# Optimization experiments

Hardware: AMD Instinct MI355X
Metric: run time of the kernel (lower is better)

The kernel has to match this reference:

```python
import jax, jax.numpy as jnp
import numpy as np

T, B, D_IN, D_H = 1024, 128, 256, 256


def setup_inputs() -> dict:
    key = jax.random.key(0)
    ks = jax.random.split(key, 9)
    s_in = 1.0 / np.sqrt(D_IN + D_H)  # torch nn.Linear init scale
    inputs = jax.random.normal(ks[0], (T, B, D_IN), dtype=jnp.float32)
    def lin(kw, kb):
        W = jax.random.uniform(kw, (D_IN + D_H, D_H), jnp.float32, -s_in, s_in)
        b = jax.random.uniform(kb, (D_H,), jnp.float32, -s_in, s_in)
        return W, b
    Wf, bf = lin(ks[1], ks[2])
    Wi, bi = lin(ks[3], ks[4])
    Wg, bg = lin(ks[5], ks[6])
    Wo, bo = lin(ks[7], ks[8])
    return {"inputs": inputs, "Wf": Wf, "bf": bf, "Wi": Wi, "bi": bi,
            "Wg": Wg, "bg": bg, "Wo": Wo, "bo": bo}


def reference(inputs, Wf, bf, Wi, bi, Wg, bg, Wo, bo):
    Bsz = inputs.shape[1]
    h0 = jnp.zeros((Bsz, D_H), inputs.dtype)
    c0 = jnp.zeros((Bsz, D_H), inputs.dtype)

    def step(carry, x):
        hx, cx = carry
        combined = jnp.concatenate([x, hx], axis=1)  # [B, D_IN+D_H]
        f = jax.nn.sigmoid(combined @ Wf + bf)
        i = jax.nn.sigmoid(combined @ Wi + bi)
        g = jnp.tanh(combined @ Wg + bg)
        o = jax.nn.sigmoid(combined @ Wo + bo)
        cx = f * cx + i * g
        hx = o * jnp.tanh(cx)
        return (hx, cx), hx

    (hx, cx), outputs = jax.lax.scan(step, (h0, c0), inputs)
    return outputs, (hx, cx)
```

## Files before the change

### kernel.cpp

```cpp
#include <hip/hip_runtime.h>
#include <hip/hip_bf16.h>

typedef short s16x8 __attribute__((ext_vector_type(8)));
typedef int   i32x4 __attribute__((ext_vector_type(4)));
typedef float f32x4 __attribute__((ext_vector_type(4)));
typedef float f32x2 __attribute__((ext_vector_type(2)));

#define T_STEPS 1024
#define BATCH   128
#define DIN     256
#define DH      256
#define NWG     64
#define NTHREADS 256

static __device__ __forceinline__ short f2bf(float f) {
  return __builtin_bit_cast(short, (__bf16)f);
}
static __device__ __forceinline__ float sigf(float x) {
  return 1.f / (1.f + __expf(-x));
}
static __device__ __forceinline__ float tanhfast(float x) {
  return 1.f - 2.f / (1.f + __expf(2.f * x));
}

static __device__ __forceinline__ i32x4 gload16_cc(const void* p) {
  i32x4 r;
  asm volatile("global_load_dwordx4 %0, %1, off sc0 sc1" : "=v"(r) : "v"(p));
  return r;
}
static __device__ __forceinline__ void gstore4_cc(void* p, unsigned v) {
  asm volatile("global_store_dword %0, %1, off sc0 sc1" :: "v"(p), "v"(v) : "memory");
}
static __device__ __forceinline__ void waitvm0_fence() {
  asm volatile("s_waitcnt vmcnt(0)" ::: "memory");
  __builtin_amdgcn_sched_barrier(0);
}

__global__ __launch_bounds__(NTHREADS, 1)
void lstm_rc(const float* __restrict__ X,
             const float* __restrict__ Wf, const float* __restrict__ bfv,
             const float* __restrict__ Wi, const float* __restrict__ biv,
             const float* __restrict__ Wg, const float* __restrict__ bgv,
             const float* __restrict__ Wo, const float* __restrict__ bov,
             float* __restrict__ out,
             unsigned short* __restrict__ hbuf,
             unsigned int* __restrict__ flags,
             int needEnd)
{
  const int bid = blockIdx.x;
  const int r   = bid & 7;
  const int csl = bid >> 3;
  const int tid = threadIdx.x;
  const int lane = tid & 63, wv = tid >> 6;
  const int grp = lane >> 4, l15 = lane & 15;
  const int r0 = r * 16;

  __shared__ short a_lds[2 * 32 * 16 * 8];
  __shared__ float elds[16 * 132];

  s16x8 bfr[2][16];
  {
    const float* Wm[4] = {Wf, Wi, Wg, Wo};
    const int gate = l15 >> 2, jj = l15 & 3;
    const float* Wsrc = Wm[gate];
#pragma unroll
    for (int n2 = 0; n2 < 2; ++n2) {
      const int ntg = wv * 2 + n2;
      const int hc  = csl * 32 + ntg * 4 + jj;
#pragma unroll
      for (int kk = 0; kk < 16; ++kk) {
        const float* p = Wsrc + (size_t)(kk * 32 + grp * 8) * DH + hc;
        s16x8 f;
#pragma unroll
        for (int s = 0; s < 8; ++s) f[s] = f2bf(p[(size_t)s * DH]);
        bfr[n2][kk] = f;
      }
    }
  }

  const int erow = tid >> 4;
  const int j2   = tid & 15;
  const int ntl  = j2 >> 1;
  const int jjl  = (j2 & 1) * 2;
  float bia[4][2];
  {
    const float* Bv[4] = {bfv, biv, bgv, bov};
#pragma unroll
    for (int g = 0; g < 4; ++g) {
      bia[g][0] = Bv[g][csl * 32 + 2 * j2];
      bia[g][1] = Bv[g][csl * 32 + 2 * j2 + 1];
    }
  }

  const int xrow = tid & 15, xseg = tid >> 4;

  f32x4 xp0, xp1, xp2, xp3;
  {
    const float* xs = X + ((size_t)0 * BATCH + r0 + xrow) * DIN + xseg * 16;
    f32x4 a = *(const f32x4*)xs, b = *(const f32x4*)(xs + 4);
    f32x4 cc = *(const f32x4*)(xs + 8), d = *(const f32x4*)(xs + 12);
    s16x8 lo, hi;
    lo[0]=f2bf(a[0]); lo[1]=f2bf(a[1]); lo[2]=f2bf(a[2]); lo[3]=f2bf(a[3]);
    lo[4]=f2bf(b[0]); lo[5]=f2bf(b[1]); lo[6]=f2bf(b[2]); lo[7]=f2bf(b[3]);
    hi[0]=f2bf(cc[0]);hi[1]=f2bf(cc[1]);hi[2]=f2bf(cc[2]);hi[3]=f2bf(cc[3]);
    hi[4]=f2bf(d[0]); hi[5]=f2bf(d[1]); hi[6]=f2bf(d[2]); hi[7]=f2bf(d[3]);
    *(s16x8*)&a_lds[((2 * xseg + 0) * 16 + xrow) * 8] = lo;
    *(s16x8*)&a_lds[((2 * xseg + 1) * 16 + xrow) * 8] = hi;
    const float* xn = X + ((size_t)1 * BATCH + r0 + xrow) * DIN + xseg * 16;
    xp0 = *(const f32x4*)xn;       xp1 = *(const f32x4*)(xn + 4);
    xp2 = *(const f32x4*)(xn + 8); xp3 = *(const f32x4*)(xn + 12);
  }
  __syncthreads();

  unsigned int* myflag = &flags[r * 32 + csl * 4 + wv];
  const unsigned int* pollp = &flags[r * 32 + (lane & 31)];
  float cs0 = 0.f, cs1 = 0.f, hO0 = 0.f, hO1 = 0.f;

  for (int t = 0; t < T_STEPS; ++t) {
    while (true) {
      unsigned fv = __hip_atomic_load(pollp, __ATOMIC_RELAXED,
                                      __HIP_MEMORY_SCOPE_AGENT);
      if (__all((int)(fv >= (unsigned)t))) break;
    }

    const unsigned short* hb = hbuf + (size_t)(t & 1) * (BATCH * DH);
    const unsigned short* hr = hb + (size_t)(r0 + l15) * DH + grp * 8;
    i32x4 hraw[8];
#pragma unroll
    for (int q = 0; q < 8; ++q) hraw[q] = gload16_cc(hr + q * 32);

    {
      short* ab = a_lds + ((t + 1) & 1) * (32 * 16 * 8);
      s16x8 lo, hi;
      lo[0]=f2bf(xp0[0]); lo[1]=f2bf(xp0[1]); lo[2]=f2bf(xp0[2]); lo[3]=f2bf(xp0[3]);
      lo[4]=f2bf(xp1[0]); lo[5]=f2bf(xp1[1]); lo[6]=f2bf(xp1[2]); lo[7]=f2bf(xp1[3]);
      hi[0]=f2bf(xp2[0]); hi[1]=f2bf(xp2[1]); hi[2]=f2bf(xp2[2]); hi[3]=f2bf(xp2[3]);
      hi[4]=f2bf(xp3[0]); hi[5]=f2bf(xp3[1]); hi[6]=f2bf(xp3[2]); hi[7]=f2bf(xp3[3]);
      *(s16x8*)&ab[((2 * xseg + 0) * 16 + xrow) * 8] = lo;
      *(s16x8*)&ab[((2 * xseg + 1) * 16 + xrow) * 8] = hi;
    }

    const short* ar = a_lds + (t & 1) * (32 * 16 * 8);
    f32x4 accx0 = {0.f,0.f,0.f,0.f}, accx1 = {0.f,0.f,0.f,0.f};
#pragma unroll
    for (int kk = 0; kk < 8; ++kk) {
      s16x8 a = *(const s16x8*)&ar[((kk * 4 + grp) * 16 + l15) * 8];
      accx0 = __builtin_amdgcn_mfma_f32_16x16x32_bf16(a, bfr[0][kk], accx0, 0, 0, 0);
      accx1 = __builtin_amdgcn_mfma_f32_16x16x32_bf16(a, bfr[1][kk], accx1, 0, 0, 0);
    }

    waitvm0_fence();
    f32x4 acch0 = {0.f,0.f,0.f,0.f}, acch1 = {0.f,0.f,0.f,0.f};
#pragma unroll
    for (int q = 0; q < 8; ++q) {
      s16x8 ah = __builtin_bit_cast(s16x8, hraw[q]);
      acch0 = __builtin_amdgcn_mfma_f32_16x16x32_bf16(ah, bfr[0][8 + q], acch0, 0, 0, 0);
      acch1 = __builtin_amdgcn_mfma_f32_16x16x32_bf16(ah, bfr[1][8 + q], acch1, 0, 0, 0);
    }
    f32x4 acc0 = accx0 + acch0, acc1 = accx1 + acch1;

    {
      const int tpre = (t + 2 < T_STEPS) ? t + 2 : T_STEPS - 1;
      const float* xs = X + ((size_t)tpre * BATCH + r0 + xrow) * DIN + xseg * 16;
      xp0 = *(const f32x4*)xs;       xp1 = *(const f32x4*)(xs + 4);
      xp2 = *(const f32x4*)(xs + 8); xp3 = *(const f32x4*)(xs + 12);
    }

#pragma unroll
    for (int rr = 0; rr < 4; ++rr) {
      elds[(grp * 4 + rr) * 132 + (wv * 2 + 0) * 16 + l15] = acc0[rr];
      elds[(grp * 4 + rr) * 132 + (wv * 2 + 1) * 16 + l15] = acc1[rr];
    }
    __syncthreads();

    const float* ez = &elds[erow * 132 + ntl * 16];
    float h0, h1;
    {
      float zf = ez[0 + jjl]  + bia[0][0];
      float zi = ez[4 + jjl]  + bia[1][0];
      float zg = ez[8 + jjl]  + bia[2][0];
      float zo = ez[12 + jjl] + bia[3][0];
      float cn = sigf(zf) * cs0 + sigf(zi) * tanhfast(zg);
      h0 = sigf(zo) * tanhfast(cn);
      cs0 = cn; hO0 = h0;
    }
    {
      float zf = ez[1 + jjl]  + bia[0][1];
      float zi = ez[5 + jjl]  + bia[1][1];
      float zg = ez[9 + jjl]  + bia[2][1];
      float zo = ez[13 + jjl] + bia[3][1];
      float cn = sigf(zf) * cs1 + sigf(zi) * tanhfast(zg);
      h1 = sigf(zo) * tanhfast(cn);
      cs1 = cn; hO1 = h1;
    }
    {
      const size_t rowg = (size_t)(r0 + erow);
      unsigned hpk = (unsigned)(unsigned short)f2bf(h0)
                   | ((unsigned)(unsigned short)f2bf(h1) << 16);
      gstore4_cc(hbuf + (size_t)((t + 1) & 1) * (BATCH * DH)
                 + rowg * DH + csl * 32 + 2 * j2, hpk);
      f32x2 ov; ov[0] = h0; ov[1] = h1;
      *(f32x2*)(out + ((size_t)t * BATCH + rowg) * DH + csl * 32 + 2 * j2) = ov;
    }

    asm volatile("s_waitcnt vmcnt(0)" ::: "memory");
    if (lane == 0)
      __hip_atomic_store(myflag, (unsigned)(t + 1), __ATOMIC_RELAXED,
                         __HIP_MEMORY_SCOPE_AGENT);
  }

  if (needEnd) {
    const unsigned int* fp = &flags[tid];
    while (__hip_atomic_load(fp, __ATOMIC_RELAXED, __HIP_MEMORY_SCOPE_AGENT)
           < (unsigned)T_STEPS) {
      __builtin_amdgcn_s_sleep(1);
    }
    __syncthreads();
  }
  {
    const size_t base = (size_t)T_STEPS * BATCH * DH;
    const size_t idx  = (size_t)(r0 + erow) * DH + csl * 32 + 2 * j2;
    out[base + idx]     = hO0;
    out[base + idx + 1] = hO1;
    out[base + BATCH * DH + idx]     = cs0;
    out[base + BATCH * DH + idx + 1] = cs1;
  }
}

extern "C" void kernel_launch(void* const* d_in, const int* in_sizes, int n_in,
                              void* d_out, int out_size, void* d_ws, size_t ws_size,
                              hipStream_t stream) {
  const float* X   = (const float*)d_in[0];
  const float* Wf  = (const float*)d_in[1];
  const float* bf_ = (const float*)d_in[2];
  const float* Wi  = (const float*)d_in[3];
  const float* bi_ = (const float*)d_in[4];
  const float* Wg  = (const float*)d_in[5];
  const float* bg_ = (const float*)d_in[6];
  const float* Wo  = (const float*)d_in[7];
  const float* bo_ = (const float*)d_in[8];
  float* out = (float*)d_out;

  const size_t hbytes = (size_t)2 * BATCH * DH * 2;
  const size_t fbytes = 2048;
  unsigned short* hbuf;
  unsigned int*   flags;
  int needEnd;
  if (ws_size >= hbytes + fbytes) {
    hbuf  = (unsigned short*)d_ws;
    flags = (unsigned int*)((unsigned char*)d_ws + hbytes);
    needEnd = 0;
    hipMemsetAsync(d_ws, 0, hbytes + fbytes, stream);
  } else {
    unsigned char* tail = (unsigned char*)d_out + (size_t)T_STEPS * BATCH * DH * 4;
    hbuf  = (unsigned short*)tail;
    flags = (unsigned int*)(tail + hbytes);
    needEnd = 1;
    hipMemsetAsync(tail, 0, hbytes + fbytes, stream);
  }

  lstm_rc<<<NWG, NTHREADS, 0, stream>>>(X, Wf, bf_, Wi, bi_, Wg, bg_,
                                        Wo, bo_, out, hbuf, flags, needEnd);
}
```

Baseline: 3.661 ms.

## Move x-projection off the critical path and use per-workgroup flags with per-wave gate exchange

The input-projection MFMAs for step t+1 are now computed after the h-store and flag publish of step t, so only the recurrent half sits between the poll and the flag write. The x-side weight fragments move to LDS to free registers. The gate exchange uses a per-wave LDS slice instead of a block-wide shuffle. One flag per workgroup, published after a block barrier, replaces per-wave flags, so pollers read 8 flags instead of 32. The cost is a __syncthreads per step before publishing, and LDS reads of the x weights every step.

```diff
diff --git a/kernel.cpp b/kernel.cpp
--- a/kernel.cpp
+++ b/kernel.cpp
@@ -16,24 +16,24 @@
 static __device__ __forceinline__ short f2bf(float f) {
   return __builtin_bit_cast(short, (__bf16)f);
 }
-static __device__ __forceinline__ float sigf(float x) {
-  return 1.f / (1.f + __expf(-x));
-}
-static __device__ __forceinline__ float tanhfast(float x) {
-  return 1.f - 2.f / (1.f + __expf(2.f * x));
-}
-
-static __device__ __forceinline__ i32x4 gload16_cc(const void* p) {
-  i32x4 r;
-  asm volatile("global_load_dwordx4 %0, %1, off sc0 sc1" : "=v"(r) : "v"(p));
+static __device__ __forceinline__ float sigf(float x){ return 1.f/(1.f+__expf(-x)); }
+static __device__ __forceinline__ float tanhfast(float x){ return 1.f - 2.f/(1.f+__expf(2.f*x)); }
+
+static __device__ __forceinline__ i32x4 ld16_cc(const void* p){
+  i32x4 r; asm volatile("global_load_dwordx4 %0, %1, off sc0 sc1" : "=v"(r) : "v"(p) : "memory"); return r;
+}
+static __device__ __forceinline__ unsigned ld4_cc(const void* p){
+  unsigned r; asm volatile("global_load_dword %0, %1, off sc0 sc1\ns_waitcnt vmcnt(0)" : "=v"(r) : "v"(p) : "memory"); return r;
+}
+static __device__ __forceinline__ void st4_cc(void* p, unsigned v){
+  asm volatile("global_store_dword %0, %1, off sc0 sc1" :: "v"(p), "v"(v) : "memory");
+}
+
+static __device__ __forceinline__ s16x8 cvt8(f32x4 a, f32x4 b){
+  s16x8 r;
+  r[0]=f2bf(a[0]); r[1]=f2bf(a[1]); r[2]=f2bf(a[2]); r[3]=f2bf(a[3]);
+  r[4]=f2bf(b[0]); r[5]=f2bf(b[1]); r[6]=f2bf(b[2]); r[7]=f2bf(b[3]);
   return r;
-}
-static __device__ __forceinline__ void gstore4_cc(void* p, unsigned v) {
-  asm volatile("global_store_dword %0, %1, off sc0 sc1" :: "v"(p), "v"(v) : "memory");
-}
-static __device__ __forceinline__ void waitvm0_fence() {
-  asm volatile("s_waitcnt vmcnt(0)" ::: "memory");
-  __builtin_amdgcn_sched_barrier(0);
 }
 
 __global__ __launch_bounds__(NTHREADS, 1)
@@ -55,173 +55,160 @@
   const int grp = lane >> 4, l15 = lane & 15;
   const int r0 = r * 16;
 
-  __shared__ short a_lds[2 * 32 * 16 * 8];
-  __shared__ float elds[16 * 132];
-
-  s16x8 bfr[2][16];
+  __shared__ short bfx[64 * 64 * 8];
+  __shared__ float elds[4 * 16 * 36];
+
+  s16x8 bh[2][8];
   {
     const float* Wm[4] = {Wf, Wi, Wg, Wo};
     const int gate = l15 >> 2, jj = l15 & 3;
     const float* Wsrc = Wm[gate];
 #pragma unroll
     for (int n2 = 0; n2 < 2; ++n2) {
-      const int ntg = wv * 2 + n2;
-      const int hc  = csl * 32 + ntg * 4 + jj;
+      const int hc = csl * 32 + (wv * 2 + n2) * 4 + jj;
 #pragma unroll
       for (int kk = 0; kk < 16; ++kk) {
         const float* p = Wsrc + (size_t)(kk * 32 + grp * 8) * DH + hc;
         s16x8 f;
 #pragma unroll
         for (int s = 0; s < 8; ++s) f[s] = f2bf(p[(size_t)s * DH]);
-        bfr[n2][kk] = f;
+        if (kk < 8) *(s16x8*)&bfx[(((wv * 2 + n2) * 8 + kk) * 64 + lane) * 8] = f;
+        else        bh[n2][kk - 8] = f;
       }
     }
   }
 
-  const int erow = tid >> 4;
-  const int j2   = tid & 15;
-  const int ntl  = j2 >> 1;
-  const int jjl  = (j2 & 1) * 2;
+  const int colg = csl * 32 + wv * 8 + 2 * grp;
   float bia[4][2];
   {
     const float* Bv[4] = {bfv, biv, bgv, bov};
 #pragma unroll
-    for (int g = 0; g < 4; ++g) {
-      bia[g][0] = Bv[g][csl * 32 + 2 * j2];
-      bia[g][1] = Bv[g][csl * 32 + 2 * j2 + 1];
-    }
-  }
-
-  const int xrow = tid & 15, xseg = tid >> 4;
-
-  f32x4 xp0, xp1, xp2, xp3;
-  {
-    const float* xs = X + ((size_t)0 * BATCH + r0 + xrow) * DIN + xseg * 16;
-    f32x4 a = *(const f32x4*)xs, b = *(const f32x4*)(xs + 4);
-    f32x4 cc = *(const f32x4*)(xs + 8), d = *(const f32x4*)(xs + 12);
-    s16x8 lo, hi;
-    lo[0]=f2bf(a[0]); lo[1]=f2bf(a[1]); lo[2]=f2bf(a[2]); lo[3]=f2bf(a[3]);
-    lo[4]=f2bf(b[0]); lo[5]=f2bf(b[1]); lo[6]=f2bf(b[2]); lo[7]=f2bf(b[3]);
-    hi[0]=f2bf(cc[0]);hi[1]=f2bf(cc[1]);hi[2]=f2bf(cc[2]);hi[3]=f2bf(cc[3]);
-    hi[4]=f2bf(d[0]); hi[5]=f2bf(d[1]); hi[6]=f2bf(d[2]); hi[7]=f2bf(d[3]);
-    *(s16x8*)&a_lds[((2 * xseg + 0) * 16 + xrow) * 8] = lo;
-    *(s16x8*)&a_lds[((2 * xseg + 1) * 16 + xrow) * 8] = hi;
-    const float* xn = X + ((size_t)1 * BATCH + r0 + xrow) * DIN + xseg * 16;
-    xp0 = *(const f32x4*)xn;       xp1 = *(const f32x4*)(xn + 4);
-    xp2 = *(const f32x4*)(xn + 8); xp3 = *(const f32x4*)(xn + 12);
+    for (int g = 0; g < 4; ++g) { bia[g][0] = Bv[g][colg]; bia[g][1] = Bv[g][colg + 1]; }
   }
   __syncthreads();
 
-  unsigned int* myflag = &flags[r * 32 + csl * 4 + wv];
-  const unsigned int* pollp = &flags[r * 32 + (lane & 31)];
-  float cs0 = 0.f, cs1 = 0.f, hO0 = 0.f, hO1 = 0.f;
+  f32x4 xr[16];
+  {
+    const float* xs0 = X + (size_t)(r0 + l15) * DIN + grp * 8;
+#pragma unroll
+    for (int kk = 0; kk < 8; ++kk) {
+      xr[2 * kk]     = *(const f32x4*)(xs0 + kk * 32);
+      xr[2 * kk + 1] = *(const f32x4*)(xs0 + kk * 32 + 4);
+    }
+  }
+  f32x4 accx0 = {0.f,0.f,0.f,0.f}, accx1 = {0.f,0.f,0.f,0.f};
+#pragma unroll
+  for (int kk = 0; kk < 8; ++kk) {
+    s16x8 fa = cvt8(xr[2 * kk], xr[2 * kk + 1]);
+    s16x8 b0 = *(const s16x8*)&bfx[(((wv * 2 + 0) * 8 + kk) * 64 + lane) * 8];
+    s16x8 b1 = *(const s16x8*)&bfx[(((wv * 2 + 1) * 8 + kk) * 64 + lane) * 8];
+    accx0 = __builtin_amdgcn_mfma_f32_16x16x32_bf16(fa, b0, accx0, 0, 0, 0);
+    accx1 = __builtin_amdgcn_mfma_f32_16x16x32_bf16(fa, b1, accx1, 0, 0, 0);
+  }
+
+  unsigned* myflag = flags + (r * 32 + csl);
+  const unsigned* pollp = flags + (r * 32 + (lane & 7));
+  float* eldsw = &elds[wv * 16 * 36];
+  float cs0 = 0.f, cs1 = 0.f, h0s = 0.f, h1s = 0.f;
 
   for (int t = 0; t < T_STEPS; ++t) {
-    while (true) {
-      unsigned fv = __hip_atomic_load(pollp, __ATOMIC_RELAXED,
-                                      __HIP_MEMORY_SCOPE_AGENT);
-      if (__all((int)(fv >= (unsigned)t))) break;
-    }
-
-    const unsigned short* hb = hbuf + (size_t)(t & 1) * (BATCH * DH);
-    const unsigned short* hr = hb + (size_t)(r0 + l15) * DH + grp * 8;
+    while (1) {
+      unsigned v = ld4_cc(pollp);
+      if (__all((int)(v >= (unsigned)t))) break;
+    }
+    __builtin_amdgcn_sched_barrier(0);
+
+    const unsigned short* hr = hbuf + (size_t)(t & 1) * (BATCH * DH)
+                             + (size_t)(r0 + l15) * DH + grp * 8;
     i32x4 hraw[8];
 #pragma unroll
-    for (int q = 0; q < 8; ++q) hraw[q] = gload16_cc(hr + q * 32);
-
-    {
-      short* ab = a_lds + ((t + 1) & 1) * (32 * 16 * 8);
-      s16x8 lo, hi;
-      lo[0]=f2bf(xp0[0]); lo[1]=f2bf(xp0[1]); lo[2]=f2bf(xp0[2]); lo[3]=f2bf(xp0[3]);
-      lo[4]=f2bf(xp1[0]); lo[5]=f2bf(xp1[1]); lo[6]=f2bf(xp1[2]); lo[7]=f2bf(xp1[3]);
-      hi[0]=f2bf(xp2[0]); hi[1]=f2bf(xp2[1]); hi[2]=f2bf(xp2[2]); hi[3]=f2bf(xp2[3]);
-      hi[4]=f2bf(xp3[0]); hi[5]=f2bf(xp3[1]); hi[6]=f2bf(xp3[2]); hi[7]=f2bf(xp3[3]);
-      *(s16x8*)&ab[((2 * xseg + 0) * 16 + xrow) * 8] = lo;
-      *(s16x8*)&ab[((2 * xseg + 1) * 16 + xrow) * 8] = hi;
-    }
-
-    const short* ar = a_lds + (t & 1) * (32 * 16 * 8);
-    f32x4 accx0 = {0.f,0.f,0.f,0.f}, accx1 = {0.f,0.f,0.f,0.f};
-#pragma unroll
-    for (int kk = 0; kk < 8; ++kk) {
-      s16x8 a = *(const s16x8*)&ar[((kk * 4 + grp) * 16 + l15) * 8];
-      accx0 = __builtin_amdgcn_mfma_f32_16x16x32_bf16(a, bfr[0][kk], accx0, 0, 0, 0);
-      accx1 = __builtin_amdgcn_mfma_f32_16x16x32_bf16(a, bfr[1][kk], accx1, 0, 0, 0);
-    }
-
-    waitvm0_fence();
-    f32x4 acch0 = {0.f,0.f,0.f,0.f}, acch1 = {0.f,0.f,0.f,0.f};
+    for (int q = 0; q < 8; ++q) hraw[q] = ld16_cc(hr + q * 32);
+    asm volatile("s_waitcnt vmcnt(0)" ::: "memory");
+    __builtin_amdgcn_sched_barrier(0);
+
+    f32x4 acc0 = accx0, acc1 = accx1;
 #pragma unroll
     for (int q = 0; q < 8; ++q) {
       s16x8 ah = __builtin_bit_cast(s16x8, hraw[q]);
-      acch0 = __builtin_amdgcn_mfma_f32_16x16x32_bf16(ah, bfr[0][8 + q], acch0, 0, 0, 0);
-      acch1 = __builtin_amdgcn_mfma_f32_16x16x32_bf16(ah, bfr[1][8 + q], acch1, 0, 0, 0);
-    }
-    f32x4 acc0 = accx0 + acch0, acc1 = accx1 + acch1;
-
-    {
-      const int tpre = (t + 2 < T_STEPS) ? t + 2 : T_STEPS - 1;
-      const float* xs = X + ((size_t)tpre * BATCH + r0 + xrow) * DIN + xseg * 16;
-      xp0 = *(const f32x4*)xs;       xp1 = *(const f32x4*)(xs + 4);
-      xp2 = *(const f32x4*)(xs + 8); xp3 = *(const f32x4*)(xs + 12);
+      acc0 = __builtin_amdgcn_mfma_f32_16x16x32_bf16(ah, bh[0][q], acc0, 0, 0, 0);
+      acc1 = __builtin_amdgcn_mfma_f32_16x16x32_bf16(ah, bh[1][q], acc1, 0, 0, 0);
     }
 
 #pragma unroll
     for (int rr = 0; rr < 4; ++rr) {
-      elds[(grp * 4 + rr) * 132 + (wv * 2 + 0) * 16 + l15] = acc0[rr];
-      elds[(grp * 4 + rr) * 132 + (wv * 2 + 1) * 16 + l15] = acc1[rr];
-    }
+      eldsw[(grp * 4 + rr) * 36 + l15]      = acc0[rr];
+      eldsw[(grp * 4 + rr) * 36 + 16 + l15] = acc1[rr];
+    }
+    asm volatile("s_waitcnt lgkmcnt(0)" ::: "memory");
+    __builtin_amdgcn_sched_barrier(0);
+    float z0[4], z1[4];
+    const int hc0 = 2 * grp, hc1 = 2 * grp + 1;
+#pragma unroll
+    for (int g = 0; g < 4; ++g) {
+      z0[g] = eldsw[l15 * 36 + ((hc0 >> 2) << 4) + 4 * g + (hc0 & 3)];
+      z1[g] = eldsw[l15 * 36 + ((hc1 >> 2) << 4) + 4 * g + (hc1 & 3)];
+    }
+
+    {
+      float zf = z0[0] + bia[0][0], zi = z0[1] + bia[1][0];
+      float zg = z0[2] + bia[2][0], zo = z0[3] + bia[3][0];
+      cs0 = sigf(zf) * cs0 + sigf(zi) * tanhfast(zg);
+      h0s = sigf(zo) * tanhfast(cs0);
+    }
+    {
+      float zf = z1[0] + bia[0][1], zi = z1[1] + bia[1][1];
+      float zg = z1[2] + bia[2][1], zo = z1[3] + bia[3][1];
+      cs1 = sigf(zf) * cs1 + sigf(zi) * tanhfast(zg);
+      h1s = sigf(zo) * tanhfast(cs1);
+    }
+
+    const int row = r0 + l15;
+    {
+      unsigned hpk = (unsigned)(unsigned short)f2bf(h0s)
+                   | ((unsigned)(unsigned short)f2bf(h1s) << 16);
+      st4_cc(hbuf + (size_t)((t + 1) & 1) * (BATCH * DH)
+             + (size_t)row * DH + colg, hpk);
+    }
+    asm volatile("s_waitcnt vmcnt(0)" ::: "memory");
     __syncthreads();
-
-    const float* ez = &elds[erow * 132 + ntl * 16];
-    float h0, h1;
-    {
-      float zf = ez[0 + jjl]  + bia[0][0];
-      float zi = ez[4 + jjl]  + bia[1][0];
-      float zg = ez[8 + jjl]  + bia[2][0];
-      float zo = ez[12 + jjl] + bia[3][0];
-      float cn = sigf(zf) * cs0 + sigf(zi) * tanhfast(zg);
-      h0 = sigf(zo) * tanhfast(cn);
-      cs0 = cn; hO0 = h0;
-    }
-    {
-      float zf = ez[1 + jjl]  + bia[0][1];
-      float zi = ez[5 + jjl]  + bia[1][1];
-      float zg = ez[9 + jjl]  + bia[2][1];
-      float zo = ez[13 + jjl] + bia[3][1];
-      float cn = sigf(zf) * cs1 + sigf(zi) * tanhfast(zg);
-      h1 = sigf(zo) * tanhfast(cn);
-      cs1 = cn; hO1 = h1;
-    }
-    {
-      const size_t rowg = (size_t)(r0 + erow);
-      unsigned hpk = (unsigned)(unsigned short)f2bf(h0)
-                   | ((unsigned)(unsigned short)f2bf(h1) << 16);
-      gstore4_cc(hbuf + (size_t)((t + 1) & 1) * (BATCH * DH)
-                 + rowg * DH + csl * 32 + 2 * j2, hpk);
-      f32x2 ov; ov[0] = h0; ov[1] = h1;
-      *(f32x2*)(out + ((size_t)t * BATCH + rowg) * DH + csl * 32 + 2 * j2) = ov;
-    }
-
-    asm volatile("s_waitcnt vmcnt(0)" ::: "memory");
-    if (lane == 0)
-      __hip_atomic_store(myflag, (unsigned)(t + 1), __ATOMIC_RELAXED,
-                         __HIP_MEMORY_SCOPE_AGENT);
+    if (tid == 0) st4_cc(myflag, (unsigned)(t + 1));
+
+    {
+      f32x2 ov; ov[0] = h0s; ov[1] = h1s;
+      *(f32x2*)(out + ((size_t)t * BATCH + row) * DH + colg) = ov;
+    }
+    {
+      const int tnx = (t + 1 < T_STEPS) ? t + 1 : T_STEPS - 1;
+      const float* xs = X + ((size_t)tnx * BATCH + r0 + l15) * DIN + grp * 8;
+#pragma unroll
+      for (int kk = 0; kk < 8; ++kk) {
+        xr[2 * kk]     = *(const f32x4*)(xs + kk * 32);
+        xr[2 * kk + 1] = *(const f32x4*)(xs + kk * 32 + 4);
+      }
+    }
+    accx0 = (f32x4){0.f,0.f,0.f,0.f}; accx1 = (f32x4){0.f,0.f,0.f,0.f};
+#pragma unroll
+    for (int kk = 0; kk < 8; ++kk) {
+      s16x8 fa = cvt8(xr[2 * kk], xr[2 * kk + 1]);
+      s16x8 b0 = *(const s16x8*)&bfx[(((wv * 2 + 0) * 8 + kk) * 64 + lane) * 8];
+      s16x8 b1 = *(const s16x8*)&bfx[(((wv * 2 + 1) * 8 + kk) * 64 + lane) * 8];
+      accx0 = __builtin_amdgcn_mfma_f32_16x16x32_bf16(fa, b0, accx0, 0, 0, 0);
+      accx1 = __builtin_amdgcn_mfma_f32_16x16x32_bf16(fa, b1, accx1, 0, 0, 0);
+    }
   }
 
   if (needEnd) {
-    const unsigned int* fp = &flags[tid];
-    while (__hip_atomic_load(fp, __ATOMIC_RELAXED, __HIP_MEMORY_SCOPE_AGENT)
-           < (unsigned)T_STEPS) {
-      __builtin_amdgcn_s_sleep(1);
+    if (wv == 0) {
+      const unsigned* fp = flags + ((lane >> 3) * 32 + (lane & 7));
+      while (ld4_cc(fp) < (unsigned)T_STEPS) __builtin_amdgcn_s_sleep(1);
     }
     __syncthreads();
   }
   {
     const size_t base = (size_t)T_STEPS * BATCH * DH;
-    const size_t idx  = (size_t)(r0 + erow) * DH + csl * 32 + 2 * j2;
-    out[base + idx]     = hO0;
-    out[base + idx + 1] = hO1;
+    const size_t idx  = (size_t)(r0 + l15) * DH + colg;
+    out[base + idx]     = h0s;
+    out[base + idx + 1] = h1s;
     out[base + BATCH * DH + idx]     = cs0;
     out[base + BATCH * DH + idx + 1] = cs1;
   }
```

New measurement: 4.414 ms. 20.5% more time.
